# Optimization experiments

Hardware: AMD Instinct MI355X
Metric: run time of the kernel (lower is better)

## Reference

```python
import jax, jax.numpy as jnp
import numpy as np

D = 768          # embed_dim
NH = 12          # num_heads
HD = D // NH     # head_dim = 64
DEPTH = 12
PATCH = 16
IMG = 256
NP_ = (IMG // PATCH) ** 2   # 256 spatial patches
PTOT = NP_ + 1              # 257 tokens per frame (cls + patches)
SCALE = HD ** -0.5
EPS = 1e-5


def _attn(xb, w, b):
    # xb: (B, S, D); w: (D, 3D); b: (3D,)
    B, S, _ = xb.shape
    qkv = (xb @ w + b).reshape(B, S, 3, NH, HD).transpose(2, 0, 3, 1, 4)
    q, k, v = qkv[0], qkv[1], qkv[2]             # each (B, NH, S, HD)
    a = jax.nn.softmax(jnp.einsum('bhqd,bhkd->bhqk', q, k) * SCALE, axis=-1)
    o = jnp.einsum('bhqk,bhkd->bhqd', a, v)      # (B, NH, S, HD)
    return o.transpose(0, 2, 1, 3).reshape(B, S, D)


def setup_inputs() -> dict:
    key = jax.random.key(0)
    ks = jax.random.split(key, 16)
    std = 0.02
    inp = {
        'x': jax.random.normal(ks[0], (2, 16, 3, IMG, IMG), jnp.float32),
        'patch_w': jax.random.normal(ks[1], (D, 3, PATCH, PATCH), jnp.float32) * std,
        'patch_b': jnp.zeros((D,), jnp.float32),
        'cls_token': jax.random.normal(ks[2], (1, 1, D), jnp.float32) * std,
        'pos_embed': jax.random.normal(ks[3], (1, PTOT, D), jnp.float32) * std,
        'time_embed': jax.random.normal(ks[4], (1, 16, D), jnp.float32) * std,
        'wqkv_s': jax.random.normal(ks[5], (DEPTH, D, 3 * D), jnp.float32) * std,
        'bqkv_s': jnp.zeros((DEPTH, 3 * D), jnp.float32),
        'wqkv_t': jax.random.normal(ks[6], (DEPTH, D, 3 * D), jnp.float32) * std,
        'bqkv_t': jnp.zeros((DEPTH, 3 * D), jnp.float32),
        'wproj': jax.random.normal(ks[7], (DEPTH, D, D), jnp.float32) * std,
        'bproj': jnp.zeros((DEPTH, D), jnp.float32),
        'ln_g': jnp.ones((D,), jnp.float32),
        'ln_b': jnp.zeros((D,), jnp.float32),
        'head_w': jax.random.normal(ks[8], (1, D), jnp.float32) * std,
        'head_b': jnp.zeros((1,), jnp.float32),
    }
    return inp


def reference(x, patch_w, patch_b, cls_token, pos_embed, time_embed,
              wqkv_s, bqkv_s, wqkv_t, bqkv_t, wproj, bproj,
              ln_g, ln_b, head_w, head_b):
    N, T, C, H, W = x.shape
    Hp = H // PATCH
    # patch embed: 16x16 stride-16 conv as unfold + matmul
    xp = x.reshape(N * T, C, Hp, PATCH, Hp, PATCH)
    xp = xp.transpose(0, 2, 4, 1, 3, 5).reshape(N * T, NP_, C * PATCH * PATCH)
    tok = xp @ patch_w.reshape(D, -1).T + patch_b          # (N*T, 256, D)
    tok = tok.reshape(N, T, NP_, D)
    cls = jnp.broadcast_to(cls_token, (N, T, 1, D))
    h = jnp.concatenate([cls, tok], axis=2)                # (N, T, 257, D)
    h = h + pos_embed[:, None]                             # (1,1,257,D) broadcast
    h = h + time_embed[:, :T][:, :, None]                  # (1,T,1,D) broadcast
    h = h.reshape(N, T * PTOT, D)

    for i in range(DEPTH):
        x4 = h.reshape(N, T, PTOT, D)
        # spatial attention within each frame
        xs = x4.reshape(N * T, PTOT, D)
        so = _attn(xs, wqkv_s[i], bqkv_s[i]) @ wproj[i] + bproj[i]
        x4 = x4 + so.reshape(N, T, PTOT, D)
        # temporal attention across frames per spatial location
        xt = x4.transpose(0, 2, 1, 3).reshape(N * PTOT, T, D)
        to = _attn(xt, wqkv_t[i], bqkv_t[i]) @ wproj[i] + bproj[i]
        x4 = x4 + to.reshape(N, PTOT, T, D).transpose(0, 2, 1, 3)
        h = x4.reshape(N, T * PTOT, D)

    mu = h.mean(axis=-1, keepdims=True)
    var = ((h - mu) ** 2).mean(axis=-1, keepdims=True)
    h = (h - mu) * jax.lax.rsqrt(var + EPS) * ln_g + ln_b
    cls_tok = h.reshape(N, T, PTOT, D)[:, :, 0, :].mean(axis=1)   # (N, D)
    logits = cls_tok @ head_w.T + head_b                          # (N, 1)
    return logits
```

## Files before the change

### kernel.cpp

```cpp
#include <hip/hip_runtime.h>
#include <hip/hip_bf16.h>
#include <math.h>

namespace {

constexpr int D    = 768;
constexpr int NH   = 12;
constexpr int PTOT = 257;
constexpr int NB   = 2;
constexpr int TT   = 16;
constexpr int NTOK = NB * TT * PTOT;
constexpr int NPAT = NB * TT * 256;
constexpr int QKVD = 3 * D;

typedef short short8  __attribute__((ext_vector_type(8)));
typedef float float4v __attribute__((ext_vector_type(4)));

__device__ __forceinline__ float bf2f(unsigned short u) {
  unsigned v = ((unsigned)u) << 16;
  float f; __builtin_memcpy(&f, &v, 4); return f;
}
__device__ __forceinline__ unsigned short f2bf(float f) {
  unsigned u; __builtin_memcpy(&u, &f, 4);
  u += 0x7FFFu + ((u >> 16) & 1u);
  return (unsigned short)(u >> 16);
}

__device__ __forceinline__ void gload_lds16(const void* g, void* l) {
  __builtin_amdgcn_global_load_lds((const __attribute__((address_space(1))) void*)g,
                                   (__attribute__((address_space(3))) void*)l, 16, 0, 0);
}

__global__ __launch_bounds__(256) void unfold_kernel(const float* __restrict__ x,
                                                     unsigned short* __restrict__ xpb) {
  int idx = blockIdx.x * 256 + threadIdx.x;
  if (idx >= NPAT * D) return;
  int f  = idx % D;
  int pg = idx / D;
  int c = f >> 8;
  int r = f & 255;
  int i = r >> 4, j = r & 15;
  int nt = pg >> 8;
  int s  = pg & 255;
  int hp = s >> 4, wp = s & 15;
  xpb[idx] = f2bf(x[(size_t)(nt * 3 + c) * 65536 + (size_t)(hp * 16 + i) * 256 + (wp * 16 + j)]);
}

__global__ __launch_bounds__(256) void cast_pw(const float* __restrict__ pw,
                                               unsigned short* __restrict__ pwb) {
  int idx = blockIdx.x * 256 + threadIdx.x;
  if (idx >= D * D) return;
  pwb[idx] = f2bf(pw[idx]);
}

__global__ __launch_bounds__(256) void wconv(const float* __restrict__ W,
                                             unsigned short* __restrict__ WT, int N) {
  __shared__ float tile[32][33];
  int l = blockIdx.z;
  const float* w = W + (size_t)l * 768 * N;
  unsigned short* wt = WT + (size_t)l * 768 * N;
  int n0 = blockIdx.x * 32, k0 = blockIdx.y * 32;
  int t = threadIdx.x;
  {
    int r = t >> 3, c4 = (t & 7) * 4;
    float4 v = *(const float4*)(w + (size_t)(k0 + r) * N + n0 + c4);
    tile[r][c4 + 0] = v.x; tile[r][c4 + 1] = v.y;
    tile[r][c4 + 2] = v.z; tile[r][c4 + 3] = v.w;
  }
  __syncthreads();
  {
    int rn = t >> 3, ck = (t & 7) * 4;
    ushort4 o;
    o.x = f2bf(tile[ck + 0][rn]); o.y = f2bf(tile[ck + 1][rn]);
    o.z = f2bf(tile[ck + 2][rn]); o.w = f2bf(tile[ck + 3][rn]);
    *(ushort4*)(wt + (size_t)(n0 + rn) * 768 + k0 + ck) = o;
  }
}

__global__ __launch_bounds__(256) void assemble_kernel(const float* __restrict__ tok,
    const float* __restrict__ cls,
    const float* __restrict__ pos, const float* __restrict__ tim,
    float* __restrict__ h, unsigned short* __restrict__ hb) {
  int idx = blockIdx.x * 256 + threadIdx.x;
  if (idx >= NTOK * D) return;
  int d = idx % D;
  int tokid = idx / D;
  int p  = tokid % PTOT;
  int nt = tokid / PTOT;
  int t  = nt % TT;
  float v = pos[p * D + d] + tim[t * D + d];
  if (p == 0) v += cls[d];
  else        v += tok[(size_t)(nt * 256 + (p - 1)) * D + d];
  h[idx] = v;
  hb[idx] = f2bf(v);
}

__global__ __launch_bounds__(256) void gemm_bf16(
    const unsigned short* __restrict__ A,
    const unsigned short* __restrict__ BT,
    const float* __restrict__ bias,
    unsigned short* __restrict__ Cb,
    float* __restrict__ Hf,
    unsigned short* __restrict__ Hb,
    int M, int N, int mode)
{
  constexpr int K = 768;
  constexpr int NT = K / 32;
  __shared__ unsigned short smem[16384];
  auto As = (unsigned short (*)[128][32])smem;
  auto Bs = (unsigned short (*)[128][32])(smem + 8192);
  auto Ct = (unsigned short (*)[128])smem;
  int tid = threadIdx.x;

  int nwg = gridDim.x * gridDim.y;
  int wg  = blockIdx.y * gridDim.x + blockIdx.x;
  int qq  = nwg >> 3, rr = nwg & 7;
  int xcd = wg & 7, bidx = wg >> 3;
  int newid = (xcd < rr ? xcd * (qq + 1) : rr * (qq + 1) + (xcd - rr) * qq) + bidx;
  int m0 = (newid / gridDim.x) * 128;
  int n0 = (newid % gridDim.x) * 128;

  int w = tid >> 6, lane = tid & 63;
  int quad = lane >> 4, l16 = lane & 15;
  int wm = (w & 1) * 64, wn = (w >> 1) * 64;
  const int lrow = lane >> 2;
  const int scol = (lane & 3) * 8;
  float4v acc[4][4] = {};

  const unsigned short* gA0 = A + (size_t)min(m0 + w * 32 + lrow, M - 1) * K + scol;
  const unsigned short* gA1 = A + (size_t)min(m0 + w * 32 + 16 + lrow, M - 1) * K + scol;
  const unsigned short* gB0 = BT + (size_t)(n0 + w * 32 + lrow) * K + scol;
  const unsigned short* gB1 = BT + (size_t)(n0 + w * 32 + 16 + lrow) * K + scol;

  auto STAGE = [&](int buf, int t) {
    int kk = t * 32;
    gload_lds16(gA0 + kk, &As[buf][w * 32][0]);
    gload_lds16(gA1 + kk, &As[buf][w * 32 + 16][0]);
    gload_lds16(gB0 + kk, &Bs[buf][w * 32][0]);
    gload_lds16(gB1 + kk, &Bs[buf][w * 32 + 16][0]);
  };
  auto COMPUTE = [&](int buf) {
    short8 af[4], bfr[4];
    #pragma unroll
    for (int i = 0; i < 4; ++i) {
      af[i]  = *(const short8*)&As[buf][wm + i * 16 + l16][quad * 8];
      bfr[i] = *(const short8*)&Bs[buf][wn + i * 16 + l16][quad * 8];
    }
    __builtin_amdgcn_s_setprio(1);
    #pragma unroll
    for (int i = 0; i < 4; ++i)
      #pragma unroll
      for (int j = 0; j < 4; ++j)
        acc[i][j] = __builtin_amdgcn_mfma_f32_16x16x32_bf16(af[i], bfr[j], acc[i][j], 0, 0, 0);
    __builtin_amdgcn_s_setprio(0);
  };

  STAGE(0, 0);
  __syncthreads();
  for (int t = 0; t < NT; t += 2) {
    STAGE(1, t + 1);
    COMPUTE(0);
    __syncthreads();
    if (t + 2 < NT) STAGE(0, t + 2);
    COMPUTE(1);
    __syncthreads();
  }

  if (mode == 2) {
    #pragma unroll
    for (int j = 0; j < 4; ++j) {
      int col = n0 + wn + j * 16 + l16;
      float bv = bias[col];
      #pragma unroll
      for (int i = 0; i < 4; ++i) {
        #pragma unroll
        for (int r = 0; r < 4; ++r) {
          int row = m0 + wm + i * 16 + quad * 4 + r;
          if (row < M) Hf[(size_t)row * N + col] = acc[i][j][r] + bv;
        }
      }
    }
    return;
  }

  #pragma unroll
  for (int j = 0; j < 4; ++j) {
    int col = wn + j * 16 + l16;
    float bv = bias[n0 + col];
    int pc = (((col >> 3) ^ quad) << 3) | (col & 7);
    #pragma unroll
    for (int i = 0; i < 4; ++i) {
      #pragma unroll
      for (int r = 0; r < 4; ++r) {
        int row = wm + i * 16 + quad * 4 + r;
        float v = acc[i][j][r] + bv;
        unsigned short ov;
        if (mode == 1) {
          size_t off = (size_t)(m0 + row) * N + (n0 + col);
          if (m0 + row < M) {
            float nv = Hf[off] + v;
            Hf[off] = nv;
            ov = f2bf(nv);
          } else ov = 0;
        } else {
          ov = f2bf(v);
        }
        Ct[row][pc] = ov;
      }
    }
  }
  __syncthreads();
  unsigned short* Ob = (mode == 0) ? Cb : Hb;
  #pragma unroll
  for (int e = 0; e < 8; ++e) {
    int c    = e * 256 + tid;
    int trow = c >> 4, tch = c & 15;
    int grow = m0 + trow;
    if (grow < M) {
      int pch = tch ^ ((trow >> 2) & 3);
      *(uint4*)(Ob + (size_t)grow * N + n0 + tch * 8) = *(const uint4*)&Ct[trow][pch * 8];
    }
  }
}

__global__ __launch_bounds__(256, 2) void attn_spatial3(
    const unsigned short* __restrict__ qkv,
    unsigned short* __restrict__ o)
{
  __shared__ unsigned short Qs[64][72];
  __shared__ unsigned short KVs[64][72];
  __shared__ unsigned short Ps[4][16][296];
  int tid = threadIdx.x;
  int w = tid >> 6, lane = tid & 63;
  int quad = lane >> 4, l16 = lane & 15;
  int bh = blockIdx.x, nt = bh / NH, head = bh % NH;
  size_t base = (size_t)nt * PTOT;
  const unsigned short* Qg = qkv + head * 64;
  const unsigned short* Kg = qkv + 768 + head * 64;
  const unsigned short* Vg = qkv + 1536 + head * 64;

  for (int q0 = 0; q0 < 320; q0 += 64) {
    __syncthreads();
    #pragma unroll
    for (int e = 0; e < 2; ++e) {
      int chunk = e * 256 + tid;
      int row = chunk >> 3, off = (chunk & 7) * 8;
      int qr = min(q0 + row, PTOT - 1);
      *(uint4*)&Qs[row][off] = *(const uint4*)(Qg + (base + qr) * (size_t)QKVD + off);
    }
    __syncthreads();
    int qrow = w * 16 + l16;
    short8 qa0 = *(const short8*)&Qs[qrow][quad * 8];
    short8 qa1 = *(const short8*)&Qs[qrow][32 + quad * 8];

    float4v st[17];
    #pragma unroll
    for (int kc = 0; kc < 5; ++kc) {
      __syncthreads();
      #pragma unroll
      for (int e = 0; e < 2; ++e) {
        int chunk = e * 256 + tid;
        int row = chunk >> 3, off = (chunk & 7) * 8;
        int kr = min(kc * 64 + row, PTOT - 1);
        *(uint4*)&KVs[row][off] = *(const uint4*)(Kg + (base + kr) * (size_t)QKVD + off);
      }
      __syncthreads();
      #pragma unroll
      for (int tt = 0; tt < 4; ++tt) {
        int t = kc * 4 + tt;
        if (t < 17) {
          short8 kb0 = *(const short8*)&KVs[tt * 16 + l16][quad * 8];
          short8 kb1 = *(const short8*)&KVs[tt * 16 + l16][32 + quad * 8];
          float4v a = {0.f, 0.f, 0.f, 0.f};
          a = __builtin_amdgcn_mfma_f32_16x16x32_bf16(qa0, kb0, a, 0, 0, 0);
          a = __builtin_amdgcn_mfma_f32_16x16x32_bf16(qa1, kb1, a, 0, 0, 0);
          st[t] = a;
        }
      }
    }
    if (l16 >= 1) {
      st[16][0] = -1e30f; st[16][1] = -1e30f; st[16][2] = -1e30f; st[16][3] = -1e30f;
    }
    float mx[4] = {-1e30f, -1e30f, -1e30f, -1e30f};
    #pragma unroll
    for (int t = 0; t < 17; ++t)
      #pragma unroll
      for (int r = 0; r < 4; ++r) mx[r] = fmaxf(mx[r], st[t][r]);
    #pragma unroll
    for (int off = 1; off < 16; off <<= 1)
      #pragma unroll
      for (int r = 0; r < 4; ++r) mx[r] = fmaxf(mx[r], __shfl_xor(mx[r], off));
    float sm[4] = {0.f, 0.f, 0.f, 0.f};
    #pragma unroll
    for (int t = 0; t < 17; ++t)
      #pragma unroll
      for (int r = 0; r < 4; ++r) {
        float e = __expf((st[t][r] - mx[r]) * 0.125f);
        st[t][r] = e;
        sm[r] += e;
      }
    #pragma unroll
    for (int off = 1; off < 16; off <<= 1)
      #pragma unroll
      for (int r = 0; r < 4; ++r) sm[r] += __shfl_xor(sm[r], off);
    float linv[4];
    #pragma unroll
    for (int r = 0; r < 4; ++r) linv[r] = 1.f / sm[r];

    #pragma unroll
    for (int t = 0; t < 17; ++t)
      #pragma unroll
      for (int r = 0; r < 4; ++r)
        Ps[w][quad * 4 + r][t * 16 + l16] = f2bf(st[t][r]);
    {
      ushort4 z = {0, 0, 0, 0};
      *(ushort4*)&Ps[w][lane >> 2][272 + (lane & 3) * 4] = z;
    }

    float4v oacc[4] = {};
    #pragma unroll
    for (int vc = 0; vc < 5; ++vc) {
      __syncthreads();
      #pragma unroll
      for (int e = 0; e < 2; ++e) {
        int chunk = e * 256 + tid;
        int row = chunk >> 3, off = (chunk & 7) * 8;
        int vr = min(vc * 64 + row, PTOT - 1);
        uint4 u = *(const uint4*)(Vg + (base + vr) * (size_t)QKVD + off);
        const unsigned short* pu = (const unsigned short*)&u;
        #pragma unroll
        for (int i = 0; i < 8; ++i) KVs[off + i][row] = pu[i];
      }
      __syncthreads();
      int ksmax = (vc == 4) ? 1 : 2;
      #pragma unroll
      for (int ks = 0; ks < 2; ++ks) {
        if (ks < ksmax) {
          int kglob = vc * 64 + ks * 32;
          short8 pa = *(const short8*)&Ps[w][l16][kglob + quad * 8];
          #pragma unroll
          for (int j = 0; j < 4; ++j) {
            short8 vb = *(const short8*)&KVs[j * 16 + l16][ks * 32 + quad * 8];
            oacc[j] = __builtin_amdgcn_mfma_f32_16x16x32_bf16(pa, vb, oacc[j], 0, 0, 0);
          }
        }
      }
    }
    #pragma unroll
    for (int r = 0; r < 4; ++r) {
      int qg = q0 + w * 16 + quad * 4 + r;
      if (qg < PTOT) {
        #pragma unroll
        for (int j = 0; j < 4; ++j)
          o[(base + qg) * (size_t)D + head * 64 + j * 16 + l16] = f2bf(oacc[j][r] * linv[r]);
      }
    }
  }
}

__global__ __launch_bounds__(256) void attn_temporal2(const unsigned short* __restrict__ qkv,
                                                      unsigned short* __restrict__ o) {
  __shared__ unsigned short Ps[4][16][32];
  __shared__ unsigned short VT[4][64][32];
  int tid = threadIdx.x;
  int w = tid >> 6, lane = tid & 63;
  int quad = lane >> 4, l16 = lane & 15;
  int s = blockIdx.x * 4 + w;
  int p  = s % PTOT;
  int nh = s / PTOT;
  int n = nh / NH, head = nh % NH;

  {
    ushort4 z = {0, 0, 0, 0};
    *(ushort4*)&Ps[w][lane >> 2][16 + (lane & 3) * 4] = z;
    *(uint4*)&VT[w][lane][16] = (uint4){0, 0, 0, 0};
    *(uint4*)&VT[w][lane][24] = (uint4){0, 0, 0, 0};
  }

  const size_t rstride = (size_t)PTOT * QKVD;
  const unsigned short* base0 = qkv + ((size_t)(n * TT) * PTOT + p) * QKVD + head * 64;

  const unsigned short* qrow = base0 + (size_t)l16 * rstride;
  short8 qa0 = *(const short8*)(qrow + quad * 8);
  short8 qa1 = *(const short8*)(qrow + 32 + quad * 8);
  const unsigned short* krow = qrow + 768;
  short8 kb0 = *(const short8*)(krow + quad * 8);
  short8 kb1 = *(const short8*)(krow + 32 + quad * 8);

  float4v sc = {0.f, 0.f, 0.f, 0.f};
  sc = __builtin_amdgcn_mfma_f32_16x16x32_bf16(qa0, kb0, sc, 0, 0, 0);
  sc = __builtin_amdgcn_mfma_f32_16x16x32_bf16(qa1, kb1, sc, 0, 0, 0);

  float e4[4], mx[4], sm[4];
  #pragma unroll
  for (int r = 0; r < 4; ++r) mx[r] = sc[r] * 0.125f;
  #pragma unroll
  for (int off = 1; off < 16; off <<= 1)
    #pragma unroll
    for (int r = 0; r < 4; ++r) mx[r] = fmaxf(mx[r], __shfl_xor(mx[r], off));
  #pragma unroll
  for (int r = 0; r < 4; ++r) { e4[r] = __expf(sc[r] * 0.125f - mx[r]); sm[r] = e4[r]; }
  #pragma unroll
  for (int off = 1; off < 16; off <<= 1)
    #pragma unroll
    for (int r = 0; r < 4; ++r) sm[r] += __shfl_xor(sm[r], off);
  float linv[4];
  #pragma unroll
  for (int r = 0; r < 4; ++r) linv[r] = 1.f / sm[r];

  #pragma unroll
  for (int r = 0; r < 4; ++r) Ps[w][quad * 4 + r][l16] = f2bf(e4[r]);

  {
    const unsigned short* vrow = qrow + 1536 + quad * 16;
    uint4 v0 = *(const uint4*)vrow;
    uint4 v1 = *(const uint4*)(vrow + 8);
    const unsigned short* pv0 = (const unsigned short*)&v0;
    const unsigned short* pv1 = (const unsigned short*)&v1;
    #pragma unroll
    for (int i = 0; i < 8; ++i) VT[w][quad * 16 + i][l16]     = pv0[i];
    #pragma unroll
    for (int i = 0; i < 8; ++i) VT[w][quad * 16 + 8 + i][l16] = pv1[i];
  }

  short8 pa = *(const short8*)&Ps[w][l16][quad * 8];
  float4v oacc[4];
  #pragma unroll
  for (int j = 0; j < 4; ++j) {
    short8 vb = *(const short8*)&VT[w][j * 16 + l16][quad * 8];
    float4v z = {0.f, 0.f, 0.f, 0.f};
    oacc[j] = __builtin_amdgcn_mfma_f32_16x16x32_bf16(pa, vb, z, 0, 0, 0);
  }

  #pragma unroll
  for (int r = 0; r < 4; ++r) {
    size_t orow = ((size_t)(n * TT + quad * 4 + r) * PTOT + p) * D + head * 64;
    #pragma unroll
    for (int j = 0; j < 4; ++j)
      o[orow + j * 16 + l16] = f2bf(oacc[j][r] * linv[r]);
  }
}

__device__ __forceinline__ float block_sum(float v, float* lds) {
  #pragma unroll
  for (int off = 32; off; off >>= 1) v += __shfl_down(v, off);
  __syncthreads();
  if ((threadIdx.x & 63) == 0) lds[threadIdx.x >> 6] = v;
  __syncthreads();
  return lds[0] + lds[1] + lds[2] + lds[3];
}

__global__ __launch_bounds__(256) void head_kernel(const float* __restrict__ h,
    const float* __restrict__ g, const float* __restrict__ b,
    const float* __restrict__ hw, const float* __restrict__ hb,
    float* __restrict__ out) {
  __shared__ float lds[4];
  int n = blockIdx.x, tid = threadIdx.x;
  float logit = 0.f;
  for (int t = 0; t < TT; ++t) {
    const float* row = h + (size_t)((n * TT + t) * PTOT) * D;
    float v[3]; float s = 0.f;
    #pragma unroll
    for (int i = 0; i < 3; ++i) { v[i] = row[tid + 256 * i]; s += v[i]; }
    s = block_sum(s, lds);
    float mu = s * (1.f / D);
    float s2 = 0.f;
    #pragma unroll
    for (int i = 0; i < 3; ++i) { float d0 = v[i] - mu; s2 += d0 * d0; }
    s2 = block_sum(s2, lds);
    float rstd = rsqrtf(s2 * (1.f / D) + 1e-5f);
    float dot = 0.f;
    #pragma unroll
    for (int i = 0; i < 3; ++i) {
      int d0 = tid + 256 * i;
      float y = (v[i] - mu) * rstd * g[d0] + b[d0];
      dot += y * hw[d0];
    }
    dot = block_sum(dot, lds);
    logit += dot;
  }
  if (tid == 0) out[n] = logit * (1.f / TT) + hb[0];
}

}

extern "C" void kernel_launch(void* const* d_in, const int* in_sizes, int n_in,
                              void* d_out, int out_size, void* d_ws, size_t ws_size,
                              hipStream_t stream) {
  const float* x       = (const float*)d_in[0];
  const float* patch_w = (const float*)d_in[1];
  const float* patch_b = (const float*)d_in[2];
  const float* cls     = (const float*)d_in[3];
  const float* pos     = (const float*)d_in[4];
  const float* tim     = (const float*)d_in[5];
  const float* wqkv_s  = (const float*)d_in[6];
  const float* bqkv_s  = (const float*)d_in[7];
  const float* wqkv_t  = (const float*)d_in[8];
  const float* bqkv_t  = (const float*)d_in[9];
  const float* wproj   = (const float*)d_in[10];
  const float* bproj   = (const float*)d_in[11];
  const float* ln_g    = (const float*)d_in[12];
  const float* ln_b    = (const float*)d_in[13];
  const float* head_w  = (const float*)d_in[14];
  const float* head_b  = (const float*)d_in[15];
  float* out = (float*)d_out;

  char* p = (char*)d_ws;
  float* h = (float*)p;                 p += (size_t)NTOK * D * 4;
  unsigned short* hb = (unsigned short*)p;   p += (size_t)NTOK * D * 2;
  unsigned short* qkvb = (unsigned short*)p; p += (size_t)NTOK * QKVD * 2;
  unsigned short* ob = (unsigned short*)p;   p += (size_t)NTOK * D * 2;
  unsigned short* wsT = (unsigned short*)p;  p += (size_t)12 * QKVD * D * 2;
  unsigned short* wtT = (unsigned short*)p;  p += (size_t)12 * QKVD * D * 2;
  unsigned short* wpT = (unsigned short*)p;  p += (size_t)12 * D * D * 2;
  unsigned short* xpb = qkvb;
  unsigned short* pwb = ob;
  float* tok = (float*)wsT;

  unfold_kernel<<<(NPAT * D + 255) / 256, 256, 0, stream>>>(x, xpb);
  cast_pw<<<(D * D + 255) / 256, 256, 0, stream>>>(patch_w, pwb);
  gemm_bf16<<<dim3(D / 128, NPAT / 128), 256, 0, stream>>>(
      xpb, pwb, patch_b, nullptr, tok, nullptr, NPAT, D, 2);
  assemble_kernel<<<(NTOK * D + 255) / 256, 256, 0, stream>>>(tok, cls, pos, tim, h, hb);

  wconv<<<dim3(QKVD / 32, D / 32, 12), 256, 0, stream>>>(wqkv_s, wsT, QKVD);
  wconv<<<dim3(QKVD / 32, D / 32, 12), 256, 0, stream>>>(wqkv_t, wtT, QKVD);
  wconv<<<dim3(D / 32, D / 32, 12), 256, 0, stream>>>(wproj, wpT, D);

  const int MB = (NTOK + 127) / 128;
  for (int l = 0; l < 12; ++l) {
    gemm_bf16<<<dim3(QKVD / 128, MB), 256, 0, stream>>>(
        hb, wsT + (size_t)l * QKVD * D, bqkv_s + (size_t)l * QKVD,
        qkvb, nullptr, nullptr, NTOK, QKVD, 0);
    attn_spatial3<<<NB * TT * NH, 256, 0, stream>>>(qkvb, ob);
    gemm_bf16<<<dim3(D / 128, MB), 256, 0, stream>>>(
        ob, wpT + (size_t)l * D * D, bproj + (size_t)l * D,
        nullptr, h, hb, NTOK, D, 1);

    gemm_bf16<<<dim3(QKVD / 128, MB), 256, 0, stream>>>(
        hb, wtT + (size_t)l * QKVD * D, bqkv_t + (size_t)l * QKVD,
        qkvb, nullptr, nullptr, NTOK, QKVD, 0);
    attn_temporal2<<<(NB * NH * PTOT) / 4, 256, 0, stream>>>(qkvb, ob);
    gemm_bf16<<<dim3(D / 128, MB), 256, 0, stream>>>(
        ob, wpT + (size_t)l * D * D, bproj + (size_t)l * D,
        nullptr, h, hb, NTOK, D, 1);
  }

  head_kernel<<<2, 256, 0, stream>>>(h, ln_g, ln_b, head_w, head_b, out);
}
```

Before: 3.073 ms.

## Split spatial attention query tiles across blocks and shrink P staging buffer

The spatial attention kernel now launches one block per (frame, head, 64-query tile) instead of looping over five query tiles inside a block, so the grid has five times as many blocks. This raises parallelism on a grid that was only 384 blocks, at the cost of reloading K and V once per query tile. The full 17-tile P buffer in shared memory is replaced by a per-chunk 64-wide buffer written inside the V loop, which cuts LDS use. The V transpose stores are rotated per thread to reduce LDS bank conflicts. The occupancy hint in launch_bounds is dropped.

```diff
diff --git a/kernel.cpp b/kernel.cpp
--- a/kernel.cpp
+++ b/kernel.cpp
@@ -223,137 +223,144 @@
   }
 }
 
-__global__ __launch_bounds__(256, 2) void attn_spatial3(
+__global__ __launch_bounds__(256) void attn_spatial3(
     const unsigned short* __restrict__ qkv,
     unsigned short* __restrict__ o)
 {
   __shared__ unsigned short Qs[64][72];
   __shared__ unsigned short KVs[64][72];
-  __shared__ unsigned short Ps[4][16][296];
+  __shared__ unsigned short Psl[4][16][72];
   int tid = threadIdx.x;
   int w = tid >> 6, lane = tid & 63;
   int quad = lane >> 4, l16 = lane & 15;
-  int bh = blockIdx.x, nt = bh / NH, head = bh % NH;
+  int bid = blockIdx.x;
+  int bh = bid / 5, qt = bid % 5;
+  int nt = bh / NH, head = bh % NH;
+  int q0 = qt * 64;
   size_t base = (size_t)nt * PTOT;
   const unsigned short* Qg = qkv + head * 64;
   const unsigned short* Kg = qkv + 768 + head * 64;
   const unsigned short* Vg = qkv + 1536 + head * 64;
 
-  for (int q0 = 0; q0 < 320; q0 += 64) {
+  #pragma unroll
+  for (int e = 0; e < 2; ++e) {
+    int chunk = e * 256 + tid;
+    int row = chunk >> 3, off = (chunk & 7) * 8;
+    int qr = min(q0 + row, PTOT - 1);
+    *(uint4*)&Qs[row][off] = *(const uint4*)(Qg + (base + qr) * (size_t)QKVD + off);
+  }
+  __syncthreads();
+  int qrow = w * 16 + l16;
+  short8 qa0 = *(const short8*)&Qs[qrow][quad * 8];
+  short8 qa1 = *(const short8*)&Qs[qrow][32 + quad * 8];
+
+  float4v st[17];
+  #pragma unroll
+  for (int kc = 0; kc < 5; ++kc) {
     __syncthreads();
     #pragma unroll
     for (int e = 0; e < 2; ++e) {
       int chunk = e * 256 + tid;
       int row = chunk >> 3, off = (chunk & 7) * 8;
-      int qr = min(q0 + row, PTOT - 1);
-      *(uint4*)&Qs[row][off] = *(const uint4*)(Qg + (base + qr) * (size_t)QKVD + off);
+      int kr = min(kc * 64 + row, PTOT - 1);
+      *(uint4*)&KVs[row][off] = *(const uint4*)(Kg + (base + kr) * (size_t)QKVD + off);
     }
     __syncthreads();
-    int qrow = w * 16 + l16;
-    short8 qa0 = *(const short8*)&Qs[qrow][quad * 8];
-    short8 qa1 = *(const short8*)&Qs[qrow][32 + quad * 8];
-
-    float4v st[17];
-    #pragma unroll
-    for (int kc = 0; kc < 5; ++kc) {
-      __syncthreads();
+    #pragma unroll
+    for (int tt = 0; tt < 4; ++tt) {
+      int t = kc * 4 + tt;
+      if (t < 17) {
+        short8 kb0 = *(const short8*)&KVs[tt * 16 + l16][quad * 8];
+        short8 kb1 = *(const short8*)&KVs[tt * 16 + l16][32 + quad * 8];
+        float4v a = {0.f, 0.f, 0.f, 0.f};
+        a = __builtin_amdgcn_mfma_f32_16x16x32_bf16(qa0, kb0, a, 0, 0, 0);
+        a = __builtin_amdgcn_mfma_f32_16x16x32_bf16(qa1, kb1, a, 0, 0, 0);
+        st[t] = a;
+      }
+    }
+  }
+  if (l16 >= 1) {
+    st[16][0] = -1e30f; st[16][1] = -1e30f; st[16][2] = -1e30f; st[16][3] = -1e30f;
+  }
+  float mx[4] = {-1e30f, -1e30f, -1e30f, -1e30f};
+  #pragma unroll
+  for (int t = 0; t < 17; ++t)
+    #pragma unroll
+    for (int r = 0; r < 4; ++r) mx[r] = fmaxf(mx[r], st[t][r]);
+  #pragma unroll
+  for (int off = 1; off < 16; off <<= 1)
+    #pragma unroll
+    for (int r = 0; r < 4; ++r) mx[r] = fmaxf(mx[r], __shfl_xor(mx[r], off));
+  float sm[4] = {0.f, 0.f, 0.f, 0.f};
+  #pragma unroll
+  for (int t = 0; t < 17; ++t)
+    #pragma unroll
+    for (int r = 0; r < 4; ++r) {
+      float e = __expf((st[t][r] - mx[r]) * 0.125f);
+      st[t][r] = e;
+      sm[r] += e;
+    }
+  #pragma unroll
+  for (int off = 1; off < 16; off <<= 1)
+    #pragma unroll
+    for (int r = 0; r < 4; ++r) sm[r] += __shfl_xor(sm[r], off);
+  float linv[4];
+  #pragma unroll
+  for (int r = 0; r < 4; ++r) linv[r] = 1.f / sm[r];
+
+  float4v oacc[4] = {};
+  #pragma unroll
+  for (int vc = 0; vc < 5; ++vc) {
+    __syncthreads();
+    #pragma unroll
+    for (int e = 0; e < 2; ++e) {
+      int chunk = e * 256 + tid;
+      int row = chunk >> 3;
+      int oo  = chunk & 7;
+      int off = oo * 8;
+      int vr = min(vc * 64 + row, PTOT - 1);
+      uint4 u = *(const uint4*)(Vg + (base + vr) * (size_t)QKVD + off);
       #pragma unroll
-      for (int e = 0; e < 2; ++e) {
-        int chunk = e * 256 + tid;
-        int row = chunk >> 3, off = (chunk & 7) * 8;
-        int kr = min(kc * 64 + row, PTOT - 1);
-        *(uint4*)&KVs[row][off] = *(const uint4*)(Kg + (base + kr) * (size_t)QKVD + off);
+      for (int s = 0; s < 8; ++s) {
+        int idx = (oo + s) & 7;
+        unsigned sel01 = (idx & 2) ? u.y : u.x;
+        unsigned sel23 = (idx & 2) ? u.w : u.z;
+        unsigned dw    = (idx & 4) ? sel23 : sel01;
+        unsigned short val = (idx & 1) ? (unsigned short)(dw >> 16) : (unsigned short)dw;
+        KVs[off + idx][row] = val;
       }
-      __syncthreads();
+    }
+    #pragma unroll
+    for (int tt = 0; tt < 4; ++tt) {
+      int t = vc * 4 + tt;
       #pragma unroll
-      for (int tt = 0; tt < 4; ++tt) {
-        int t = kc * 4 + tt;
-        if (t < 17) {
-          short8 kb0 = *(const short8*)&KVs[tt * 16 + l16][quad * 8];
-          short8 kb1 = *(const short8*)&KVs[tt * 16 + l16][32 + quad * 8];
-          float4v a = {0.f, 0.f, 0.f, 0.f};
-          a = __builtin_amdgcn_mfma_f32_16x16x32_bf16(qa0, kb0, a, 0, 0, 0);
-          a = __builtin_amdgcn_mfma_f32_16x16x32_bf16(qa1, kb1, a, 0, 0, 0);
-          st[t] = a;
+      for (int r = 0; r < 4; ++r) {
+        unsigned short pv = 0;
+        if (t < 17) pv = f2bf(st[t][r]);
+        Psl[w][quad * 4 + r][tt * 16 + l16] = pv;
+      }
+    }
+    __syncthreads();
+    int ksmax = (vc == 4) ? 1 : 2;
+    #pragma unroll
+    for (int ks = 0; ks < 2; ++ks) {
+      if (ks < ksmax) {
+        short8 pa = *(const short8*)&Psl[w][l16][ks * 32 + quad * 8];
+        #pragma unroll
+        for (int j = 0; j < 4; ++j) {
+          short8 vb = *(const short8*)&KVs[j * 16 + l16][ks * 32 + quad * 8];
+          oacc[j] = __builtin_amdgcn_mfma_f32_16x16x32_bf16(pa, vb, oacc[j], 0, 0, 0);
         }
       }
     }
-    if (l16 >= 1) {
-      st[16][0] = -1e30f; st[16][1] = -1e30f; st[16][2] = -1e30f; st[16][3] = -1e30f;
-    }
-    float mx[4] = {-1e30f, -1e30f, -1e30f, -1e30f};
-    #pragma unroll
-    for (int t = 0; t < 17; ++t)
+  }
+  #pragma unroll
+  for (int r = 0; r < 4; ++r) {
+    int qg = q0 + w * 16 + quad * 4 + r;
+    if (qg < PTOT) {
       #pragma unroll
-      for (int r = 0; r < 4; ++r) mx[r] = fmaxf(mx[r], st[t][r]);
-    #pragma unroll
-    for (int off = 1; off < 16; off <<= 1)
-      #pragma unroll
-      for (int r = 0; r < 4; ++r) mx[r] = fmaxf(mx[r], __shfl_xor(mx[r], off));
-    float sm[4] = {0.f, 0.f, 0.f, 0.f};
-    #pragma unroll
-    for (int t = 0; t < 17; ++t)
-      #pragma unroll
-      for (int r = 0; r < 4; ++r) {
-        float e = __expf((st[t][r] - mx[r]) * 0.125f);
-        st[t][r] = e;
-        sm[r] += e;
-      }
-    #pragma unroll
-    for (int off = 1; off < 16; off <<= 1)
-      #pragma unroll
-      for (int r = 0; r < 4; ++r) sm[r] += __shfl_xor(sm[r], off);
-    float linv[4];
-    #pragma unroll
-    for (int r = 0; r < 4; ++r) linv[r] = 1.f / sm[r];
-
-    #pragma unroll
-    for (int t = 0; t < 17; ++t)
-      #pragma unroll
-      for (int r = 0; r < 4; ++r)
-        Ps[w][quad * 4 + r][t * 16 + l16] = f2bf(st[t][r]);
-    {
-      ushort4 z = {0, 0, 0, 0};
-      *(ushort4*)&Ps[w][lane >> 2][272 + (lane & 3) * 4] = z;
-    }
-
-    float4v oacc[4] = {};
-    #pragma unroll
-    for (int vc = 0; vc < 5; ++vc) {
-      __syncthreads();
-      #pragma unroll
-      for (int e = 0; e < 2; ++e) {
-        int chunk = e * 256 + tid;
-        int row = chunk >> 3, off = (chunk & 7) * 8;
-        int vr = min(vc * 64 + row, PTOT - 1);
-        uint4 u = *(const uint4*)(Vg + (base + vr) * (size_t)QKVD + off);
-        const unsigned short* pu = (const unsigned short*)&u;
-        #pragma unroll
-        for (int i = 0; i < 8; ++i) KVs[off + i][row] = pu[i];
-      }
-      __syncthreads();
-      int ksmax = (vc == 4) ? 1 : 2;
-      #pragma unroll
-      for (int ks = 0; ks < 2; ++ks) {
-        if (ks < ksmax) {
-          int kglob = vc * 64 + ks * 32;
-          short8 pa = *(const short8*)&Ps[w][l16][kglob + quad * 8];
-          #pragma unroll
-          for (int j = 0; j < 4; ++j) {
-            short8 vb = *(const short8*)&KVs[j * 16 + l16][ks * 32 + quad * 8];
-            oacc[j] = __builtin_amdgcn_mfma_f32_16x16x32_bf16(pa, vb, oacc[j], 0, 0, 0);
-          }
-        }
-      }
-    }
-    #pragma unroll
-    for (int r = 0; r < 4; ++r) {
-      int qg = q0 + w * 16 + quad * 4 + r;
-      if (qg < PTOT) {
-        #pragma unroll
-        for (int j = 0; j < 4; ++j)
-          o[(base + qg) * (size_t)D + head * 64 + j * 16 + l16] = f2bf(oacc[j][r] * linv[r]);
-      }
+      for (int j = 0; j < 4; ++j)
+        o[(base + qg) * (size_t)D + head * 64 + j * 16 + l16] = f2bf(oacc[j][r] * linv[r]);
     }
   }
 }
@@ -532,7 +539,7 @@
     gemm_bf16<<<dim3(QKVD / 128, MB), 256, 0, stream>>>(
         hb, wsT + (size_t)l * QKVD * D, bqkv_s + (size_t)l * QKVD,
         qkvb, nullptr, nullptr, NTOK, QKVD, 0);
-    attn_spatial3<<<NB * TT * NH, 256, 0, stream>>>(qkvb, ob);
+    attn_spatial3<<<NB * TT * NH * 5, 256, 0, stream>>>(qkvb, ob);
     gemm_bf16<<<dim3(D / 128, MB), 256, 0, stream>>>(
         ob, wpT + (size_t)l * D * D, bproj + (size_t)l * D,
         nullptr, h, hb, NTOK, D, 1);
```

Result: faster. 2.867 ms (-6.7%).
